# Kernel optimization log

Measured on AMD Instinct MI355X. Metric: run time of the kernel, lower is better.

Reference implementation:

```python
import jax, jax.numpy as jnp
import numpy as np

B, S, C, H = 4, 2048, 256, 8  # batch, seq, hidden_dim (== per-head dim), n_heads


def setup_inputs() -> dict:
    key = jax.random.key(0)
    ks = jax.random.split(key, 9)
    sc_in = 1.0 / np.sqrt(C)
    sc_out = 1.0 / np.sqrt(C * H)
    return {
        "x":  jax.random.normal(ks[0], (B, S, C), dtype=jnp.float32),
        "Wq": jax.random.normal(ks[1], (C, C * H), dtype=jnp.float32) * sc_in,
        "bq": jax.random.normal(ks[2], (C * H,), dtype=jnp.float32) * 0.01,
        "Wk": jax.random.normal(ks[3], (C, C * H), dtype=jnp.float32) * sc_in,
        "bk": jax.random.normal(ks[4], (C * H,), dtype=jnp.float32) * 0.01,
        "Wv": jax.random.normal(ks[5], (C, C * H), dtype=jnp.float32) * sc_in,
        "bv": jax.random.normal(ks[6], (C * H,), dtype=jnp.float32) * 0.01,
        "Wo": jax.random.normal(ks[7], (C * H, C), dtype=jnp.float32) * sc_out,
        "bo": jax.random.normal(ks[8], (C,), dtype=jnp.float32) * 0.01,
    }


def reference(x, Wq, bq, Wk, bk, Wv, bv, Wo, bo):
    b, s, c = x.shape
    h = H
    # projections: (b, s, c) -> (b, s, h, c); per-head dim equals full hidden dim c
    q = (x @ Wq + bq).reshape(b, s, h, c)
    k = (x @ Wk + bk).reshape(b, s, h, c)
    v = (x @ Wv + bv).reshape(b, s, h, c)
    # scale q and k each by c**(-1/4) == total scale 1/sqrt(c)
    scale = jnp.asarray(c, x.dtype) ** -0.25
    q = q * scale
    k = k * scale
    # attention scores: (b, h, s_q, s_k)
    scores = jnp.einsum("bqhc,bkhc->bhqk", q, k)
    weights = jax.nn.softmax(scores, axis=-1)  # softmax over keys (torch dim=2 on (b*h, sq, sk))
    out = jnp.einsum("bhqk,bkhc->bqhc", weights, v).reshape(b, s, h * c)
    return out @ Wo + bo
```

## Files before the change

kernel.cpp:

```cpp
#include <hip/hip_runtime.h>
#include <stdint.h>
#include <math.h>

#define B_ 4
#define S_ 2048
#define C_ 256
#define H_ 8

typedef short bf16x8 __attribute__((ext_vector_type(8)));
typedef float f32x4 __attribute__((ext_vector_type(4)));
typedef float f32x16 __attribute__((ext_vector_type(16)));

static __device__ __forceinline__ short f2bf(float f) {
  uint32_t u = __float_as_uint(f);
  u = (u + 0x7fffu + ((u >> 16) & 1u)) >> 16;
  return (short)u;
}

static __device__ __forceinline__ int cvtpk(float lo, float hi) {
  int r;
  asm("v_cvt_pk_bf16_f32 %0, %1, %2" : "=v"(r) : "v"(lo), "v"(hi));
  return r;
}

static __device__ __forceinline__ bf16x8 pack4(int a, int b, int c, int d) {
  union { int i[4]; bf16x8 v; } u;
  u.i[0] = a; u.i[1] = b; u.i[2] = c; u.i[3] = d;
  return u.v;
}

static __device__ __forceinline__ void gld16(const void* g, void* l) {
  __builtin_amdgcn_global_load_lds(
      (const __attribute__((address_space(1))) uint32_t*)g,
      (__attribute__((address_space(3))) uint32_t*)l, 16, 0, 0);
}

__global__ void cvt_f32_bf16(const float* __restrict__ in, short* __restrict__ out, int n) {
  int i = (blockIdx.x * 256 + threadIdx.x) * 8;
  if (i >= n) return;
  float4 a = *(const float4*)(in + i);
  float4 b = *(const float4*)(in + i + 4);
  bf16x8 r;
  r[0] = f2bf(a.x); r[1] = f2bf(a.y); r[2] = f2bf(a.z); r[3] = f2bf(a.w);
  r[4] = f2bf(b.x); r[5] = f2bf(b.y); r[6] = f2bf(b.z); r[7] = f2bf(b.w);
  *(bf16x8*)(out + i) = r;
}

__global__ void transpose_cvt(const float* __restrict__ in, short* __restrict__ out,
                              int R, int Cc) {
  __shared__ float t[32][33];
  int cb = blockIdx.x * 32, rb = blockIdx.y * 32;
  int tr = threadIdx.x >> 5;
  int tc = threadIdx.x & 31;
#pragma unroll
  for (int i = 0; i < 4; i++)
    t[tr + i * 8][tc] = in[(size_t)(rb + tr + i * 8) * Cc + cb + tc];
  __syncthreads();
#pragma unroll
  for (int i = 0; i < 4; i++)
    out[(size_t)(cb + tr + i * 8) * R + rb + tc] = f2bf(t[tc][tr + i * 8]);
}

template<int MODE>
__global__ void __launch_bounds__(256, 2) gemm_k(
    const short* __restrict__ A, const short* __restrict__ Bt,
    const float* __restrict__ bias, float scale, void* __restrict__ out,
    int M, int N, int K) {
  __shared__ char smem[36864];
  const int tid = threadIdx.x;
  const int l = tid & 63;
  const int w = tid >> 6;
  const int wr = w >> 1, wc = w & 1;
  const int mbase = blockIdx.y * 128;
  const int nbase = blockIdx.x * 128;

  const f32x4 fzero = {0.f, 0.f, 0.f, 0.f};
  f32x4 acc[4][4];
#pragma unroll
  for (int i = 0; i < 4; i++)
#pragma unroll
    for (int j = 0; j < 4; j++) acc[i][j] = fzero;

  const int nkt = K >> 5;
  for (int kt = 0; kt < nkt; ++kt) {
#pragma unroll
    for (int c = 0; c < 2; c++) {
      int row = c * 64 + w * 16 + (l >> 2);
      const short* ga = A + (size_t)(mbase + row) * K + kt * 32 + (l & 3) * 8;
      gld16(ga, smem + (c * 4 + w) * 1024);
      const short* gb = Bt + (size_t)(nbase + row) * K + kt * 32 + (l & 3) * 8;
      gld16(gb, smem + 8192 + (c * 4 + w) * 1024);
    }
    __syncthreads();
    bf16x8 af[4], bf[4];
#pragma unroll
    for (int mf = 0; mf < 4; mf++)
      af[mf] = *(const bf16x8*)(smem + (wr * 64 + mf * 16 + (l & 15)) * 64 + ((l >> 4) << 4));
#pragma unroll
    for (int nf = 0; nf < 4; nf++)
      bf[nf] = *(const bf16x8*)(smem + 8192 + (wc * 64 + nf * 16 + (l & 15)) * 64 + ((l >> 4) << 4));
#pragma unroll
    for (int mf = 0; mf < 4; mf++)
#pragma unroll
      for (int nf = 0; nf < 4; nf++)
        acc[mf][nf] = __builtin_amdgcn_mfma_f32_16x16x32_bf16(af[mf], bf[nf], acc[mf][nf], 0, 0, 0);
    __syncthreads();
  }

  if (MODE == 0) {
#pragma unroll
    for (int mf = 0; mf < 4; mf++)
#pragma unroll
      for (int nf = 0; nf < 4; nf++)
#pragma unroll
        for (int i = 0; i < 4; i++) {
          int m = mbase + wr * 64 + mf * 16 + (l >> 4) * 4 + i;
          int n = nbase + wc * 64 + nf * 16 + (l & 15);
          float v = (acc[mf][nf][i] + bias[n]) * scale;
          int b = m >> 11, s = m & 2047;
          int h = n >> 8, d = n & 255;
          ((short*)out)[((size_t)(b * H_ + h) * S_ + s) * C_ + d] = f2bf(v);
        }
  } else if (MODE == 2) {
#pragma unroll
    for (int mf = 0; mf < 4; mf++)
#pragma unroll
      for (int nf = 0; nf < 4; nf++)
#pragma unroll
        for (int i = 0; i < 4; i++) {
          int m = mbase + wr * 64 + mf * 16 + (l >> 4) * 4 + i;
          int n = nbase + wc * 64 + nf * 16 + (l & 15);
          ((float*)out)[(size_t)m * N + n] = acc[mf][nf][i] + bias[n];
        }
  } else {
    short* T = (short*)smem;
#pragma unroll
    for (int mf = 0; mf < 4; mf++)
#pragma unroll
      for (int nf = 0; nf < 4; nf++)
#pragma unroll
        for (int i = 0; i < 4; i++) {
          int ml = wr * 64 + mf * 16 + (l >> 4) * 4 + i;
          int nl = wc * 64 + nf * 16 + (l & 15);
          float v = (acc[mf][nf][i] + bias[nbase + nl]) * scale;
          T[ml * 136 + nl] = f2bf(v);
        }
    __syncthreads();
    int b = mbase >> 11, s0 = mbase & 2047;
    int h = nbase >> 8;
    int kt0 = s0 >> 5;
    char* hb = (char*)out + ((size_t)(b * H_ + h) << 20);
    if (MODE == 3) {
#pragma unroll
      for (int i2 = 0; i2 < 8; i2++) {
        int sid = tid * 8 + i2;
        int kt_l = sid >> 9, rem = sid & 511;
        int ksl = rem >> 6, lane2 = rem & 63;
        int tok = kt_l * 32 + (lane2 & 31);
        int dl = ksl * 16 + ((lane2 >> 5) << 3);
        bf16x8 v = *(const bf16x8*)&T[tok * 136 + dl];
        int ksg = ((nbase & 255) >> 4) + ksl;
        *(bf16x8*)(hb + ((size_t)(kt0 + kt_l) << 14) + ((ksg * 64 + lane2) << 4)) = v;
      }
    } else {
#pragma unroll
      for (int i2 = 0; i2 < 8; i2++) {
        int sid = tid * 8 + i2;
        int kt_l = sid >> 9, rem = sid & 511;
        int dtl = rem >> 7, kb = (rem >> 6) & 1, lane2 = rem & 63;
        int dl = dtl * 32 + (lane2 & 31);
        int k0 = kt_l * 32 + kb * 16 + ((lane2 >> 5) << 3);
        bf16x8 pk;
#pragma unroll
        for (int j = 0; j < 8; j++) pk[j] = T[(k0 + j) * 136 + dl];
        int dtg = ((nbase & 255) >> 5) + dtl;
        *(bf16x8*)(hb + ((size_t)(kt0 + kt_l) << 14) + (((dtg * 2 + kb) * 64 + lane2) << 4)) = pk;
      }
    }
  }
}

__global__ void __launch_bounds__(256, 2) attn_k(
    const short* __restrict__ Qg, const char* __restrict__ Kpk,
    const char* __restrict__ Vpk, short* __restrict__ Ag) {
  __shared__ char smem[65536];
  const int tid = threadIdx.x, l = tid & 63, w = tid >> 6;
  const int hi = l >> 5;
  const int lq = l & 31;

  const int orig = (blockIdx.x & 7) * 64 + (blockIdx.x >> 3);
  const int head = orig >> 4;
  const int qbase = (orig & 15) * 128 + w * 32;

  bf16x8 qf[16];
  {
    const short* qb = Qg + ((size_t)head * S_ + qbase + lq) * C_;
#pragma unroll
    for (int ks = 0; ks < 16; ks++) {
      qf[ks] = *(const bf16x8*)(qb + ks * 16 + hi * 8);
      asm volatile("" : "+v"(qf[ks]));
    }
  }

  f32x16 o[8];
#pragma unroll
  for (int dt = 0; dt < 8; dt++)
#pragma unroll
    for (int r = 0; r < 16; r++) o[dt][r] = 0.0f;
  float lrun = 0.0f;

  const char* kpH = Kpk + ((size_t)head << 20);
  const char* vpH = Vpk + ((size_t)head << 20);
  const int vo = tid << 4;
  const int lo = l << 4;

  auto STAGE = [&](int t) {
    char* Kd = smem + (t & 1) * 32768;
    char* Vd = Kd + 16384;
    const char* kq = kpH + ((size_t)t << 14);
    const char* vq = vpH + ((size_t)t << 14);
#pragma unroll
    for (int c = 0; c < 4; c++)
      gld16(kq + c * 4096 + vo, Kd + c * 4096 + vo);
#pragma unroll
    for (int c = 0; c < 4; c++)
      gld16(vq + c * 4096 + vo, Vd + c * 4096 + vo);
  };

  auto CALC = [&](int t) {
    const char* Ks = smem + (t & 1) * 32768;
    const char* Vs = Ks + 16384;
    f32x16 st;
#pragma unroll
    for (int r = 0; r < 16; r++) st[r] = 0.0f;
#pragma unroll
    for (int ks = 0; ks < 16; ks++) {
      bf16x8 kf = *(const bf16x8*)(Ks + ks * 1024 + lo);
      st = __builtin_amdgcn_mfma_f32_32x32x16_bf16(kf, qf[ks], st, 0, 0, 0);
    }
#pragma unroll
    for (int r = 0; r < 16; r++) st[r] = exp2f(st[r]);
    {
      float t0 = (st[0] + st[1]) + (st[2] + st[3]);
      float t1 = (st[4] + st[5]) + (st[6] + st[7]);
      float t2 = (st[8] + st[9]) + (st[10] + st[11]);
      float t3 = (st[12] + st[13]) + (st[14] + st[15]);
      lrun += (t0 + t1) + (t2 + t3);
    }
    {
      int a0 = cvtpk(st[0], st[1]), a1 = cvtpk(st[2], st[3]);
      int a2 = cvtpk(st[4], st[5]), a3 = cvtpk(st[6], st[7]);
      auto s0p = __builtin_amdgcn_permlane32_swap(a0, a2, false, false);
      auto s1p = __builtin_amdgcn_permlane32_swap(a1, a3, false, false);
      bf16x8 pf0 = pack4(s0p[0], s1p[0], s0p[1], s1p[1]);
#pragma unroll
      for (int dt = 0; dt < 8; dt++) {
        bf16x8 v0 = *(const bf16x8*)(Vs + (dt * 2) * 1024 + lo);
        o[dt] = __builtin_amdgcn_mfma_f32_32x32x16_bf16(v0, pf0, o[dt], 0, 0, 0);
      }
    }
    {
      int a4 = cvtpk(st[8], st[9]),   a5 = cvtpk(st[10], st[11]);
      int a6 = cvtpk(st[12], st[13]), a7 = cvtpk(st[14], st[15]);
      auto s2p = __builtin_amdgcn_permlane32_swap(a4, a6, false, false);
      auto s3p = __builtin_amdgcn_permlane32_swap(a5, a7, false, false);
      bf16x8 pf1 = pack4(s2p[0], s3p[0], s2p[1], s3p[1]);
#pragma unroll
      for (int dt = 0; dt < 8; dt++) {
        bf16x8 v1 = *(const bf16x8*)(Vs + (dt * 2 + 1) * 1024 + lo);
        o[dt] = __builtin_amdgcn_mfma_f32_32x32x16_bf16(v1, pf1, o[dt], 0, 0, 0);
      }
    }
  };

  STAGE(0);

#pragma unroll 1
  for (int t = 0; t < 64; ++t) {
    if (t < 63) {
      STAGE(t + 1);
      asm volatile("s_waitcnt vmcnt(8)" ::: "memory");
    } else {
      asm volatile("s_waitcnt vmcnt(0)" ::: "memory");
    }
    __builtin_amdgcn_s_barrier();
    CALC(t);
    asm volatile("" ::: "memory");
    __builtin_amdgcn_s_barrier();
  }

  float lsum = lrun + __shfl_xor(lrun, 32);
  float inv = 1.0f / lsum;
  char* ob = smem + w * 16384;
#pragma unroll
  for (int dt = 0; dt < 8; dt++) {
#pragma unroll
    for (int m = 0; m < 4; m++) {
      int lo32 = cvtpk(o[dt][4 * m + 0] * inv, o[dt][4 * m + 1] * inv);
      int hi32 = cvtpk(o[dt][4 * m + 2] * inv, o[dt][4 * m + 3] * inv);
      int cs = (dt * 4 + m) ^ lq;
      int* p = (int*)(ob + lq * 512 + cs * 16 + hi * 8);
      p[0] = lo32; p[1] = hi32;
    }
  }
  int bb = head >> 3, hh = head & 7;
#pragma unroll
  for (int pi = 0; pi < 16; pi++) {
    int qr = pi * 2 + hi;
    bf16x8 v = *(const bf16x8*)(ob + qr * 512 + ((lq ^ qr) << 4));
    size_t g = ((size_t)(bb * S_ + qbase + qr) * (H_ * C_)) + hh * C_ + lq * 8;
    *(bf16x8*)(Ag + g) = v;
  }
}

extern "C" void kernel_launch(void* const* d_in, const int* in_sizes, int n_in,
                              void* d_out, int out_size, void* d_ws, size_t ws_size,
                              hipStream_t stream) {
  const float* x  = (const float*)d_in[0];
  const float* Wq = (const float*)d_in[1];
  const float* bq = (const float*)d_in[2];
  const float* Wk = (const float*)d_in[3];
  const float* bk = (const float*)d_in[4];
  const float* Wv = (const float*)d_in[5];
  const float* bv = (const float*)d_in[6];
  const float* Wo = (const float*)d_in[7];
  const float* bo = (const float*)d_in[8];

  char* ws = (char*)d_ws;
  short* xb  = (short*)(ws);
  short* WqT = (short*)(ws + 4194304);
  short* WkT = (short*)(ws + 5242880);
  short* WvT = (short*)(ws + 6291456);
  short* WoT = (short*)(ws + 7340032);
  short* Qg  = (short*)(ws + 8388608);
  char*  Kpk = (char*)(ws + 41943040);
  char*  Vpk = (char*)(ws + 75497472);
  short* Ag  = (short*)(ws + 109051904);

  cvt_f32_bf16<<<1024, 256, 0, stream>>>(x, xb, 8192 * 256);
  transpose_cvt<<<dim3(64, 8), 256, 0, stream>>>(Wq, WqT, 256, 2048);
  transpose_cvt<<<dim3(64, 8), 256, 0, stream>>>(Wk, WkT, 256, 2048);
  transpose_cvt<<<dim3(64, 8), 256, 0, stream>>>(Wv, WvT, 256, 2048);
  transpose_cvt<<<dim3(8, 64), 256, 0, stream>>>(Wo, WoT, 2048, 256);

  const float scq = 0.25f * 1.44269504088896f;
  const float sck = 0.25f;
  gemm_k<0><<<dim3(16, 64), 256, 0, stream>>>(xb, WqT, bq, scq, Qg, 8192, 2048, 256);
  gemm_k<3><<<dim3(16, 64), 256, 0, stream>>>(xb, WkT, bk, sck, Kpk, 8192, 2048, 256);
  gemm_k<1><<<dim3(16, 64), 256, 0, stream>>>(xb, WvT, bv, 1.0f, Vpk, 8192, 2048, 256);
  attn_k<<<512, 256, 0, stream>>>(Qg, Kpk, Vpk, Ag);
  gemm_k<2><<<dim3(2, 64), 256, 0, stream>>>(Ag, WoT, bo, 1.0f, (float*)d_out, 8192, 256, 2048);
}
```

Measured before the change: 265.1 us.

## Deepen attention pipeline, split-K output projection, merge weight transposes

The attention kernel now runs 512-thread blocks covering 256 queries and uses a 4-slot, 128KB LDS ring with a prefetch distance of two tiles. It also drops the trailing barrier per iteration and raises wave priority around the MFMA sections, all to hide K/V load latency better. The output projection is split over K into 4 partial GEMMs written to the freed K buffer, followed by a reduction kernel that adds the bias; this gives the small 128-block GEMM more parallelism at the cost of extra memory traffic. The four weight-transpose launches are merged into a single launch to cut launch overhead.

```diff
diff --git a/kernel.cpp b/kernel.cpp
--- a/kernel.cpp
+++ b/kernel.cpp
@@ -46,10 +46,23 @@
   *(bf16x8*)(out + i) = r;
 }
 
-__global__ void transpose_cvt(const float* __restrict__ in, short* __restrict__ out,
-                              int R, int Cc) {
+__global__ void transpose_cvt4(const float* __restrict__ Wq, const float* __restrict__ Wk,
+                               const float* __restrict__ Wv, const float* __restrict__ Wo,
+                               short* __restrict__ WqT, short* __restrict__ WkT,
+                               short* __restrict__ WvT, short* __restrict__ WoT) {
   __shared__ float t[32][33];
-  int cb = blockIdx.x * 32, rb = blockIdx.y * 32;
+  int bid = blockIdx.x;
+  int which = bid >> 9, rem = bid & 511;
+  const float* in; short* outp; int R, Cc, bx, by;
+  if (which < 3) {
+    R = 256; Cc = 2048; bx = rem & 63; by = rem >> 6;
+    in = which == 0 ? Wq : (which == 1 ? Wk : Wv);
+    outp = which == 0 ? WqT : (which == 1 ? WkT : WvT);
+  } else {
+    R = 2048; Cc = 256; bx = rem & 7; by = rem >> 3;
+    in = Wo; outp = WoT;
+  }
+  int cb = bx * 32, rb = by * 32;
   int tr = threadIdx.x >> 5;
   int tc = threadIdx.x & 31;
 #pragma unroll
@@ -58,7 +71,7 @@
   __syncthreads();
 #pragma unroll
   for (int i = 0; i < 4; i++)
-    out[(size_t)(cb + tr + i * 8) * R + rb + tc] = f2bf(t[tc][tr + i * 8]);
+    outp[(size_t)(cb + tr + i * 8) * R + rb + tc] = f2bf(t[tc][tr + i * 8]);
 }
 
 template<int MODE>
@@ -81,8 +94,9 @@
 #pragma unroll
     for (int j = 0; j < 4; j++) acc[i][j] = fzero;
 
-  const int nkt = K >> 5;
-  for (int kt = 0; kt < nkt; ++kt) {
+  const int kt0 = (MODE == 4) ? blockIdx.z * 16 : 0;
+  const int nkt = (MODE == 4) ? 16 : (K >> 5);
+  for (int kt = kt0; kt < kt0 + nkt; ++kt) {
 #pragma unroll
     for (int c = 0; c < 2; c++) {
       int row = c * 64 + w * 16 + (l >> 2);
@@ -121,7 +135,8 @@
           int h = n >> 8, d = n & 255;
           ((short*)out)[((size_t)(b * H_ + h) * S_ + s) * C_ + d] = f2bf(v);
         }
-  } else if (MODE == 2) {
+  } else if (MODE == 4) {
+    float* pout = (float*)out + (size_t)blockIdx.z * M * N;
 #pragma unroll
     for (int mf = 0; mf < 4; mf++)
 #pragma unroll
@@ -130,7 +145,7 @@
         for (int i = 0; i < 4; i++) {
           int m = mbase + wr * 64 + mf * 16 + (l >> 4) * 4 + i;
           int n = nbase + wc * 64 + nf * 16 + (l & 15);
-          ((float*)out)[(size_t)m * N + n] = acc[mf][nf][i] + bias[n];
+          pout[(size_t)m * N + n] = acc[mf][nf][i];
         }
   } else {
     short* T = (short*)smem;
@@ -148,7 +163,7 @@
     __syncthreads();
     int b = mbase >> 11, s0 = mbase & 2047;
     int h = nbase >> 8;
-    int kt0 = s0 >> 5;
+    int kt0e = s0 >> 5;
     char* hb = (char*)out + ((size_t)(b * H_ + h) << 20);
     if (MODE == 3) {
 #pragma unroll
@@ -160,7 +175,7 @@
         int dl = ksl * 16 + ((lane2 >> 5) << 3);
         bf16x8 v = *(const bf16x8*)&T[tok * 136 + dl];
         int ksg = ((nbase & 255) >> 4) + ksl;
-        *(bf16x8*)(hb + ((size_t)(kt0 + kt_l) << 14) + ((ksg * 64 + lane2) << 4)) = v;
+        *(bf16x8*)(hb + ((size_t)(kt0e + kt_l) << 14) + ((ksg * 64 + lane2) << 4)) = v;
       }
     } else {
 #pragma unroll
@@ -174,23 +189,41 @@
 #pragma unroll
         for (int j = 0; j < 8; j++) pk[j] = T[(k0 + j) * 136 + dl];
         int dtg = ((nbase & 255) >> 5) + dtl;
-        *(bf16x8*)(hb + ((size_t)(kt0 + kt_l) << 14) + (((dtg * 2 + kb) * 64 + lane2) << 4)) = pk;
+        *(bf16x8*)(hb + ((size_t)(kt0e + kt_l) << 14) + (((dtg * 2 + kb) * 64 + lane2) << 4)) = pk;
       }
     }
   }
 }
 
-__global__ void __launch_bounds__(256, 2) attn_k(
+__global__ void reduce4(const float* __restrict__ part, const float* __restrict__ bias,
+                        float* __restrict__ out) {
+  const int MN = 8192 * 256;
+  int i = (blockIdx.x * 256 + threadIdx.x) * 4;
+  if (i >= MN) return;
+  float4 a = *(const float4*)(part + i);
+  float4 b = *(const float4*)(part + MN + i);
+  float4 c = *(const float4*)(part + 2 * MN + i);
+  float4 d = *(const float4*)(part + 3 * MN + i);
+  float4 bs = *(const float4*)(bias + (i & 255));
+  float4 r;
+  r.x = a.x + b.x + c.x + d.x + bs.x;
+  r.y = a.y + b.y + c.y + d.y + bs.y;
+  r.z = a.z + b.z + c.z + d.z + bs.z;
+  r.w = a.w + b.w + c.w + d.w + bs.w;
+  *(float4*)(out + i) = r;
+}
+
+__global__ void __launch_bounds__(512, 2) attn_k(
     const short* __restrict__ Qg, const char* __restrict__ Kpk,
     const char* __restrict__ Vpk, short* __restrict__ Ag) {
-  __shared__ char smem[65536];
+  __shared__ char smem[131072];
   const int tid = threadIdx.x, l = tid & 63, w = tid >> 6;
   const int hi = l >> 5;
   const int lq = l & 31;
 
-  const int orig = (blockIdx.x & 7) * 64 + (blockIdx.x >> 3);
-  const int head = orig >> 4;
-  const int qbase = (orig & 15) * 128 + w * 32;
+  const int orig = (blockIdx.x & 7) * 32 + (blockIdx.x >> 3);
+  const int head = orig >> 3;
+  const int qbase = (orig & 7) * 256 + w * 32;
 
   bf16x8 qf[16];
   {
@@ -215,29 +248,31 @@
   const int lo = l << 4;
 
   auto STAGE = [&](int t) {
-    char* Kd = smem + (t & 1) * 32768;
+    char* Kd = smem + (t & 3) * 32768;
     char* Vd = Kd + 16384;
     const char* kq = kpH + ((size_t)t << 14);
     const char* vq = vpH + ((size_t)t << 14);
 #pragma unroll
-    for (int c = 0; c < 4; c++)
-      gld16(kq + c * 4096 + vo, Kd + c * 4096 + vo);
-#pragma unroll
-    for (int c = 0; c < 4; c++)
-      gld16(vq + c * 4096 + vo, Vd + c * 4096 + vo);
+    for (int c = 0; c < 2; c++)
+      gld16(kq + c * 8192 + vo, Kd + c * 8192 + vo);
+#pragma unroll
+    for (int c = 0; c < 2; c++)
+      gld16(vq + c * 8192 + vo, Vd + c * 8192 + vo);
   };
 
   auto CALC = [&](int t) {
-    const char* Ks = smem + (t & 1) * 32768;
+    const char* Ks = smem + (t & 3) * 32768;
     const char* Vs = Ks + 16384;
     f32x16 st;
 #pragma unroll
     for (int r = 0; r < 16; r++) st[r] = 0.0f;
+    __builtin_amdgcn_s_setprio(1);
 #pragma unroll
     for (int ks = 0; ks < 16; ks++) {
       bf16x8 kf = *(const bf16x8*)(Ks + ks * 1024 + lo);
       st = __builtin_amdgcn_mfma_f32_32x32x16_bf16(kf, qf[ks], st, 0, 0, 0);
     }
+    __builtin_amdgcn_s_setprio(0);
 #pragma unroll
     for (int r = 0; r < 16; r++) st[r] = exp2f(st[r]);
     {
@@ -247,6 +282,7 @@
       float t3 = (st[12] + st[13]) + (st[14] + st[15]);
       lrun += (t0 + t1) + (t2 + t3);
     }
+    __builtin_amdgcn_s_setprio(1);
     {
       int a0 = cvtpk(st[0], st[1]), a1 = cvtpk(st[2], st[3]);
       int a2 = cvtpk(st[4], st[5]), a3 = cvtpk(st[6], st[7]);
@@ -271,23 +307,26 @@
         o[dt] = __builtin_amdgcn_mfma_f32_32x32x16_bf16(v1, pf1, o[dt], 0, 0, 0);
       }
     }
+    __builtin_amdgcn_s_setprio(0);
   };
 
   STAGE(0);
+  STAGE(1);
 
 #pragma unroll 1
-  for (int t = 0; t < 64; ++t) {
-    if (t < 63) {
-      STAGE(t + 1);
-      asm volatile("s_waitcnt vmcnt(8)" ::: "memory");
-    } else {
-      asm volatile("s_waitcnt vmcnt(0)" ::: "memory");
-    }
+  for (int t = 0; t < 62; ++t) {
+    STAGE(t + 2);
+    asm volatile("s_waitcnt vmcnt(8)" ::: "memory");
     __builtin_amdgcn_s_barrier();
     CALC(t);
-    asm volatile("" ::: "memory");
-    __builtin_amdgcn_s_barrier();
-  }
+  }
+  asm volatile("s_waitcnt vmcnt(4)" ::: "memory");
+  __builtin_amdgcn_s_barrier();
+  CALC(62);
+  asm volatile("s_waitcnt vmcnt(0)" ::: "memory");
+  __builtin_amdgcn_s_barrier();
+  CALC(63);
+  __builtin_amdgcn_s_barrier();
 
   float lsum = lrun + __shfl_xor(lrun, 32);
   float inv = 1.0f / lsum;
@@ -338,16 +377,14 @@
   short* Ag  = (short*)(ws + 109051904);
 
   cvt_f32_bf16<<<1024, 256, 0, stream>>>(x, xb, 8192 * 256);
-  transpose_cvt<<<dim3(64, 8), 256, 0, stream>>>(Wq, WqT, 256, 2048);
-  transpose_cvt<<<dim3(64, 8), 256, 0, stream>>>(Wk, WkT, 256, 2048);
-  transpose_cvt<<<dim3(64, 8), 256, 0, stream>>>(Wv, WvT, 256, 2048);
-  transpose_cvt<<<dim3(8, 64), 256, 0, stream>>>(Wo, WoT, 2048, 256);
+  transpose_cvt4<<<2048, 256, 0, stream>>>(Wq, Wk, Wv, Wo, WqT, WkT, WvT, WoT);
 
   const float scq = 0.25f * 1.44269504088896f;
   const float sck = 0.25f;
   gemm_k<0><<<dim3(16, 64), 256, 0, stream>>>(xb, WqT, bq, scq, Qg, 8192, 2048, 256);
   gemm_k<3><<<dim3(16, 64), 256, 0, stream>>>(xb, WkT, bk, sck, Kpk, 8192, 2048, 256);
   gemm_k<1><<<dim3(16, 64), 256, 0, stream>>>(xb, WvT, bv, 1.0f, Vpk, 8192, 2048, 256);
-  attn_k<<<512, 256, 0, stream>>>(Qg, Kpk, Vpk, Ag);
-  gemm_k<2><<<dim3(2, 64), 256, 0, stream>>>(Ag, WoT, bo, 1.0f, (float*)d_out, 8192, 256, 2048);
-}
+  attn_k<<<256, 512, 0, stream>>>(Qg, Kpk, Vpk, Ag);
+  gemm_k<4><<<dim3(2, 64, 4), 256, 0, stream>>>(Ag, WoT, nullptr, 1.0f, Kpk, 8192, 256, 2048);
+  reduce4<<<2048, 256, 0, stream>>>((const float*)Kpk, bo, (float*)d_out);
+}
```

After: 247.8 us. 1.07x faster.
